# Kernel tuning notes

Measured on AMD Instinct MI355X. Metric: run time of the kernel, lower is better.

Reference implementation:

```python
import jax, jax.numpy as jnp
import numpy as np

EMBED = 100
BATCH = 4096
NUM_NEG = 256
U, P, W, RP, B, C = 30000, 50000, 100000, 50000, 5000, 1000


def _tab(k, v, e=EMBED):
    r = 0.5 / e
    w = jax.random.uniform(k, (v + 1, e), minval=-r, maxval=r, dtype=jnp.float32)
    return w.at[-1].set(0.0)  # padding row is zeros, as in torch code


def setup_inputs() -> dict:
    key = jax.random.key(0)
    ks = jax.random.split(key, 10)
    inp = {
        'user_emb': _tab(ks[0], U),
        'product_emb': _tab(ks[1], P),
        'word_emb': _tab(ks[2], W),
        'brand_emb': _tab(ks[3], B),
        'category_emb': _tab(ks[4], C),
        'rproduct_emb': _tab(ks[5], RP),
        'rel_vecs': jax.random.uniform(ks[6], (8, EMBED), minval=-0.5 / EMBED, maxval=0.5 / EMBED, dtype=jnp.float32),
        'purchase_bias': jnp.zeros((P + 1,), jnp.float32),
        'mentions_bias': jnp.zeros((W + 1,), jnp.float32),
        'describe_bias': jnp.zeros((W + 1,), jnp.float32),
        'produced_bias': jnp.zeros((B + 1,), jnp.float32),
        'belongs_bias': jnp.zeros((C + 1,), jnp.float32),
        'also_bought_bias': jnp.zeros((RP + 1,), jnp.float32),
        'also_viewed_bias': jnp.zeros((RP + 1,), jnp.float32),
        'together_bias': jnp.zeros((RP + 1,), jnp.float32),
    }
    # batch_idxs columns: (u, p, w, b, c, rp1, rp2, rp3), each in its own vocab range
    col_max = [U, P, W, B, C, RP, RP, RP]
    cols = [jax.random.randint(jax.random.fold_in(ks[7], i), (BATCH,), 0, m) for i, m in enumerate(col_max)]
    inp['batch_idxs'] = jnp.stack(cols, axis=1)
    # deterministic stand-in for torch.multinomial negative sampling, one row per relation
    neg_max = [P, W, W, B, C, RP, RP, RP]
    negs = [jax.random.randint(jax.random.fold_in(ks[8], i), (NUM_NEG,), 0, m) for i, m in enumerate(neg_max)]
    inp['neg_idxs'] = jnp.stack(negs, axis=0)
    return inp


def _neg_loss(head_tab, tail_tab, rvec, bias_tab, h, t, n):
    hv = head_tab[h]                      # [B,E] gather
    ex = hv + rvec                        # [B,E]
    tv = tail_tab[t]                      # [B,E]
    bias = bias_tab[t]                    # [B]
    pos = jnp.sum(ex * tv, axis=-1) + bias  # bmm([B,1,E],[B,E,1]) == rowwise dot
    nv = tail_tab[n]                      # [N,E]
    neg = jnp.einsum('be,ne->bn', ex, nv) + bias[:, None]  # [B,N]
    pos_loss = -jax.nn.log_sigmoid(pos)   # == -log(sigmoid(pos)), stable
    neg_loss = -jax.nn.log_sigmoid(-neg).sum(axis=1)
    return (pos_loss + neg_loss).mean()


def reference(batch_idxs, neg_idxs, user_emb, product_emb, word_emb, brand_emb,
              category_emb, rproduct_emb, rel_vecs, purchase_bias, mentions_bias,
              describe_bias, produced_bias, belongs_bias, also_bought_bias,
              also_viewed_bias, together_bias):
    # (head_tab, tail_tab, bias_tab, head_col, tail_col) per relation, in original order
    rels = [
        (user_emb, product_emb, purchase_bias, 0, 1),
        (user_emb, word_emb, mentions_bias, 0, 2),
        (product_emb, word_emb, describe_bias, 1, 2),
        (product_emb, brand_emb, produced_bias, 1, 3),
        (product_emb, category_emb, belongs_bias, 1, 4),
        (product_emb, rproduct_emb, also_bought_bias, 1, 5),
        (product_emb, rproduct_emb, also_viewed_bias, 1, 6),
        (product_emb, rproduct_emb, together_bias, 1, 7),
    ]
    loss = jnp.float32(0.0)
    for r, (ht, tt, bt, hc, tc) in enumerate(rels):
        loss = loss + _neg_loss(ht, tt, rel_vecs[r], bt,
                                batch_idxs[:, hc], batch_idxs[:, tc], neg_idxs[r])
    return loss
```

## Files before the change

### kernel.cpp

```cpp
#include <hip/hip_runtime.h>


#define EMBED   100
#define BATCH   4096
#define NUM_NEG 256
#define BM      64
#define BN      128
#define PITCH   104

typedef __attribute__((ext_vector_type(8))) short s8;
typedef __attribute__((ext_vector_type(4))) float f4;

struct RelP {
    const float* head;
    const float* tail;
    const float* bias;
    int hc, tc;
};

struct Params {
    RelP rel[8];
    const float* rel_vecs;
    const int*   batch_idxs;
    const int*   neg_idxs;
    float*       out;
};

__device__ __forceinline__ float softplus_f(float x) {
    float e = __expf(-fabsf(x));
    return fmaxf(x, 0.0f) + __logf(1.0f + e);
}

__device__ __forceinline__ unsigned short bf16_rne(float f) {
    unsigned u = __float_as_uint(f);
    u += 0x7FFFu + ((u >> 16) & 1u);
    return (unsigned short)(u >> 16);
}

__device__ __forceinline__ float bf16_to_f(short s) {
    return __uint_as_float(((unsigned)(unsigned short)s) << 16);
}

__device__ __forceinline__ s8 pack8(float4 f0, float4 f1) {
    s8 v = { (short)bf16_rne(f0.x), (short)bf16_rne(f0.y),
             (short)bf16_rne(f0.z), (short)bf16_rne(f0.w),
             (short)bf16_rne(f1.x), (short)bf16_rne(f1.y),
             (short)bf16_rne(f1.z), (short)bf16_rne(f1.w) };
    return v;
}

__launch_bounds__(256, 4)
__global__ void ke_kernel(Params p) {
    const int bid = blockIdx.x;
    const int r   = bid & 7;
    const int x   = bid >> 3;
    const int rb  = x & 63;
    const int nb  = x >> 6;
    const int tid = threadIdx.x;

    __shared__ __align__(16) short As[BM * PITCH];
    __shared__ __align__(16) short Bs[BN * PITCH];

    const RelP rp = p.rel[r];

    if (tid < BM) {
        const int row  = tid;
        const int grow = rb * BM + row;
        const int h  = p.batch_idxs[grow * 8 + rp.hc];
        const int ti = p.batch_idxs[grow * 8 + rp.tc];
        const float4* s4p = (const float4*)(rp.head + (size_t)h * EMBED);
        const float4* rv4 = (const float4*)(p.rel_vecs + r * EMBED);
        const unsigned short extra = bf16_rne(rp.bias[ti]);
        short* dst = As + row * PITCH;
#pragma unroll
        for (int c = 0; c < 12; ++c) {
            float4 f0 = s4p[2 * c];
            float4 f1 = s4p[2 * c + 1];
            const float4 a = rv4[2 * c];
            const float4 b = rv4[2 * c + 1];
            f0.x += a.x; f0.y += a.y; f0.z += a.z; f0.w += a.w;
            f1.x += b.x; f1.y += b.y; f1.z += b.z; f1.w += b.w;
            *(s8*)(dst + 8 * c) = pack8(f0, f1);
        }
        {
            float4 f = s4p[24];
            const float4 a = rv4[24];
            f.x += a.x; f.y += a.y; f.z += a.z; f.w += a.w;
            s8 v = { (short)bf16_rne(f.x), (short)bf16_rne(f.y),
                     (short)bf16_rne(f.z), (short)bf16_rne(f.w),
                     (short)extra, 0, 0, 0 };
            *(s8*)(dst + 96) = v;
        }
    } else if (tid < 192) {
        const int row = tid - 64;
        const int n = p.neg_idxs[r * NUM_NEG + nb * BN + row];
        const float4* s4p = (const float4*)(rp.tail + (size_t)n * EMBED);
        short* dst = Bs + row * PITCH;
#pragma unroll
        for (int c = 0; c < 12; ++c) {
            float4 f0 = s4p[2 * c];
            float4 f1 = s4p[2 * c + 1];
            *(s8*)(dst + 8 * c) = pack8(f0, f1);
        }
        {
            float4 f = s4p[24];
            s8 v = { (short)bf16_rne(f.x), (short)bf16_rne(f.y),
                     (short)bf16_rne(f.z), (short)bf16_rne(f.w),
                     (short)0x3F80, 0, 0, 0 };
            *(s8*)(dst + 96) = v;
        }
    }

    const bool doPos = tid >= 128;
    const float* ptail = rp.tail;
    float pbias = 0.0f;
    if (doPos) {
        const int pl   = tid - 128;
        const int prow = rb * BM + nb * 32 + (pl >> 2);
        const int pt   = p.batch_idxs[prow * 8 + rp.tc];
        ptail = rp.tail + (size_t)pt * EMBED;
        pbias = rp.bias[pt];
    }

    __syncthreads();

    const int wave = tid >> 6;
    const int lane = tid & 63;
    const int li   = lane & 15;
    const int q    = lane >> 4;
    const int wm   = wave >> 1;
    const int wn   = wave & 1;

    f4 acc[2][4];
#pragma unroll
    for (int i = 0; i < 2; ++i)
#pragma unroll
        for (int j = 0; j < 4; ++j)
            acc[i][j] = (f4){0.f, 0.f, 0.f, 0.f};

    const short* Ab = As + (wm * 32 + li) * PITCH;
    const short* Bb = Bs + (wn * 64 + li) * PITCH;

#pragma unroll
    for (int s = 0; s < 3; ++s) {
        const int co = 8 * (q + 4 * s);
        s8 a[2], b[4];
        a[0] = *(const s8*)(Ab + co);
        a[1] = *(const s8*)(Ab + 16 * PITCH + co);
        b[0] = *(const s8*)(Bb + co);
        b[1] = *(const s8*)(Bb + 16 * PITCH + co);
        b[2] = *(const s8*)(Bb + 32 * PITCH + co);
        b[3] = *(const s8*)(Bb + 48 * PITCH + co);
#pragma unroll
        for (int i = 0; i < 2; ++i)
#pragma unroll
            for (int j = 0; j < 4; ++j)
                acc[i][j] = __builtin_amdgcn_mfma_f32_16x16x32_bf16(a[i], b[j], acc[i][j], 0, 0, 0);
    }
    {
        const s8 z = {0, 0, 0, 0, 0, 0, 0, 0};
        s8 a[2], b[4];
        a[0] = *(const s8*)(Ab + 96);
        a[1] = *(const s8*)(Ab + 16 * PITCH + 96);
        b[0] = *(const s8*)(Bb + 96);
        b[1] = *(const s8*)(Bb + 16 * PITCH + 96);
        b[2] = *(const s8*)(Bb + 32 * PITCH + 96);
        b[3] = *(const s8*)(Bb + 48 * PITCH + 96);
        b[0] = q ? z : b[0];
        b[1] = q ? z : b[1];
        b[2] = q ? z : b[2];
        b[3] = q ? z : b[3];
#pragma unroll
        for (int i = 0; i < 2; ++i)
#pragma unroll
            for (int j = 0; j < 4; ++j)
                acc[i][j] = __builtin_amdgcn_mfma_f32_16x16x32_bf16(a[i], b[j], acc[i][j], 0, 0, 0);
    }

    float local = 0.0f;
#pragma unroll
    for (int i = 0; i < 2; ++i)
#pragma unroll
        for (int j = 0; j < 4; ++j) {
            local += softplus_f(acc[i][j].x);
            local += softplus_f(acc[i][j].y);
            local += softplus_f(acc[i][j].z);
            local += softplus_f(acc[i][j].w);
        }

    if (doPos) {
        const int pl   = tid - 128;
        const int prl  = pl >> 2;
        const int part = pl & 3;
        const short* exr = As + (nb * 32 + prl) * PITCH;
        const float4* tv = (const float4*)ptail;
        float d0 = 0.f, d1 = 0.f, d2 = 0.f, d3 = 0.f;
        const int cbase = 3 * part;
#pragma unroll
        for (int k = 0; k < 3; ++k) {
            const int c = cbase + k;
            const s8 e = *(const s8*)(exr + 8 * c);
            const float4 t0 = tv[2 * c];
            const float4 t1 = tv[2 * c + 1];
            d0 = fmaf(bf16_to_f(e[0]), t0.x, d0);
            d1 = fmaf(bf16_to_f(e[1]), t0.y, d1);
            d2 = fmaf(bf16_to_f(e[2]), t0.z, d2);
            d3 = fmaf(bf16_to_f(e[3]), t0.w, d3);
            d0 = fmaf(bf16_to_f(e[4]), t1.x, d0);
            d1 = fmaf(bf16_to_f(e[5]), t1.y, d1);
            d2 = fmaf(bf16_to_f(e[6]), t1.z, d2);
            d3 = fmaf(bf16_to_f(e[7]), t1.w, d3);
        }
        if (part == 3) {
            const s8 e = *(const s8*)(exr + 96);
            const float4 t0 = tv[24];
            d0 = fmaf(bf16_to_f(e[0]), t0.x, d0);
            d1 = fmaf(bf16_to_f(e[1]), t0.y, d1);
            d2 = fmaf(bf16_to_f(e[2]), t0.z, d2);
            d3 = fmaf(bf16_to_f(e[3]), t0.w, d3);
        }
        float d = (d0 + d1) + (d2 + d3);
        d += __shfl_xor(d, 1, 64);
        d += __shfl_xor(d, 2, 64);
        if (part == 0) local += softplus_f(-(d + pbias));
    }

#pragma unroll
    for (int off = 32; off > 0; off >>= 1)
        local += __shfl_down(local, off, 64);

    __syncthreads();
    float* wsum = (float*)Bs;
    if ((tid & 63) == 0) wsum[tid >> 6] = local;
    __syncthreads();
    if (tid == 0) {
        const float s = (wsum[0] + wsum[1]) + (wsum[2] + wsum[3]);
        atomicAdd(p.out, s * (1.0f / BATCH));
    }
}

extern "C" void kernel_launch(void* const* d_in, const int* in_sizes, int n_in,
                              void* d_out, int out_size, void* d_ws, size_t ws_size,
                              hipStream_t stream) {
    const float* user  = (const float*)d_in[0];
    const float* prod  = (const float*)d_in[1];
    const float* word  = (const float*)d_in[2];
    const float* brand = (const float*)d_in[3];
    const float* cat   = (const float*)d_in[4];
    const float* rprod = (const float*)d_in[5];

    Params p;
    p.rel_vecs   = (const float*)d_in[6];
    p.batch_idxs = (const int*)d_in[15];
    p.neg_idxs   = (const int*)d_in[16];
    p.out        = (float*)d_out;

    p.rel[0] = {user, prod,  (const float*)d_in[7],  0, 1};
    p.rel[1] = {user, word,  (const float*)d_in[8],  0, 2};
    p.rel[2] = {prod, word,  (const float*)d_in[9],  1, 2};
    p.rel[3] = {prod, brand, (const float*)d_in[10], 1, 3};
    p.rel[4] = {prod, cat,   (const float*)d_in[11], 1, 4};
    p.rel[5] = {prod, rprod, (const float*)d_in[12], 1, 5};
    p.rel[6] = {prod, rprod, (const float*)d_in[13], 1, 6};
    p.rel[7] = {prod, rprod, (const float*)d_in[14], 1, 7};

    hipMemsetAsync(d_out, 0, sizeof(float), stream);
    ke_kernel<<<1024, 256, 0, stream>>>(p);
}
```

Before: 153.8 us.

## Cover all negatives per block and spread gather loads across all threads

Each block now handles all 256 negative samples for its 64-row batch tile (BN 256, grid halved to 512). This removes the duplicate gather and conversion of the head rows across the two former column blocks. The global-to-LDS gather is restructured so all 256 threads participate, with 8 threads per row each loading float4 chunks, instead of one thread per row serially loading 100 floats. The positive-score dot product is spread across all threads in 4-way groups. The trade-offs are a larger accumulator per wave (16 MFMA tiles), fewer blocks resident (launch bounds 2), and more LDS per block.

Result: no change. 152.2 us (median of 2 runs) (-1.0%).

```diff
diff --git a/kernel.cpp b/kernel.cpp
--- a/kernel.cpp
+++ b/kernel.cpp
@@ -5,10 +5,11 @@
 #define BATCH   4096
 #define NUM_NEG 256
 #define BM      64
-#define BN      128
+#define BN      256
 #define PITCH   104
 
 typedef __attribute__((ext_vector_type(8))) short s8;
+typedef __attribute__((ext_vector_type(4))) short s4;
 typedef __attribute__((ext_vector_type(4))) float f4;
 
 struct RelP {
@@ -41,21 +42,17 @@
     return __uint_as_float(((unsigned)(unsigned short)s) << 16);
 }
 
-__device__ __forceinline__ s8 pack8(float4 f0, float4 f1) {
-    s8 v = { (short)bf16_rne(f0.x), (short)bf16_rne(f0.y),
-             (short)bf16_rne(f0.z), (short)bf16_rne(f0.w),
-             (short)bf16_rne(f1.x), (short)bf16_rne(f1.y),
-             (short)bf16_rne(f1.z), (short)bf16_rne(f1.w) };
+__device__ __forceinline__ s4 pack4(float4 f) {
+    s4 v = { (short)bf16_rne(f.x), (short)bf16_rne(f.y),
+             (short)bf16_rne(f.z), (short)bf16_rne(f.w) };
     return v;
 }
 
-__launch_bounds__(256, 4)
+__launch_bounds__(256, 2)
 __global__ void ke_kernel(Params p) {
     const int bid = blockIdx.x;
     const int r   = bid & 7;
-    const int x   = bid >> 3;
-    const int rb  = x & 63;
-    const int nb  = x >> 6;
+    const int rb  = bid >> 3;
     const int tid = threadIdx.x;
 
     __shared__ __align__(16) short As[BM * PITCH];
@@ -63,26 +60,28 @@
 
     const RelP rp = p.rel[r];
 
-    if (tid < BM) {
-        const int row  = tid;
+    const int g    = tid & 7;
+    const int rloc = tid >> 3;
+
+    const float4* rv4 = (const float4*)(p.rel_vecs + r * EMBED);
+#pragma unroll
+    for (int pass = 0; pass < 2; ++pass) {
+        const int row  = pass * 32 + rloc;
         const int grow = rb * BM + row;
-        const int h  = p.batch_idxs[grow * 8 + rp.hc];
-        const int ti = p.batch_idxs[grow * 8 + rp.tc];
+        const int h = p.batch_idxs[grow * 8 + rp.hc];
         const float4* s4p = (const float4*)(rp.head + (size_t)h * EMBED);
-        const float4* rv4 = (const float4*)(p.rel_vecs + r * EMBED);
-        const unsigned short extra = bf16_rne(rp.bias[ti]);
         short* dst = As + row * PITCH;
 #pragma unroll
-        for (int c = 0; c < 12; ++c) {
-            float4 f0 = s4p[2 * c];
-            float4 f1 = s4p[2 * c + 1];
-            const float4 a = rv4[2 * c];
-            const float4 b = rv4[2 * c + 1];
-            f0.x += a.x; f0.y += a.y; f0.z += a.z; f0.w += a.w;
-            f1.x += b.x; f1.y += b.y; f1.z += b.z; f1.w += b.w;
-            *(s8*)(dst + 8 * c) = pack8(f0, f1);
-        }
-        {
+        for (int t = 0; t < 3; ++t) {
+            const int j = g + 8 * t;
+            float4 f = s4p[j];
+            const float4 a = rv4[j];
+            f.x += a.x; f.y += a.y; f.z += a.z; f.w += a.w;
+            *(s4*)(dst + 4 * j) = pack4(f);
+        }
+        if (g == 0) {
+            const int ti = p.batch_idxs[grow * 8 + rp.tc];
+            const unsigned short extra = bf16_rne(rp.bias[ti]);
             float4 f = s4p[24];
             const float4 a = rv4[24];
             f.x += a.x; f.y += a.y; f.z += a.z; f.w += a.w;
@@ -91,18 +90,20 @@
                      (short)extra, 0, 0, 0 };
             *(s8*)(dst + 96) = v;
         }
-    } else if (tid < 192) {
-        const int row = tid - 64;
-        const int n = p.neg_idxs[r * NUM_NEG + nb * BN + row];
+    }
+
+#pragma unroll
+    for (int pass = 0; pass < 8; ++pass) {
+        const int row = pass * 32 + rloc;
+        const int n = p.neg_idxs[r * NUM_NEG + row];
         const float4* s4p = (const float4*)(rp.tail + (size_t)n * EMBED);
         short* dst = Bs + row * PITCH;
 #pragma unroll
-        for (int c = 0; c < 12; ++c) {
-            float4 f0 = s4p[2 * c];
-            float4 f1 = s4p[2 * c + 1];
-            *(s8*)(dst + 8 * c) = pack8(f0, f1);
-        }
-        {
+        for (int t = 0; t < 3; ++t) {
+            const int j = g + 8 * t;
+            *(s4*)(dst + 4 * j) = pack4(s4p[j]);
+        }
+        if (g == 0) {
             float4 f = s4p[24];
             s8 v = { (short)bf16_rne(f.x), (short)bf16_rne(f.y),
                      (short)bf16_rne(f.z), (short)bf16_rne(f.w),
@@ -111,16 +112,12 @@
         }
     }
 
-    const bool doPos = tid >= 128;
-    const float* ptail = rp.tail;
-    float pbias = 0.0f;
-    if (doPos) {
-        const int pl   = tid - 128;
-        const int prow = rb * BM + nb * 32 + (pl >> 2);
-        const int pt   = p.batch_idxs[prow * 8 + rp.tc];
-        ptail = rp.tail + (size_t)pt * EMBED;
-        pbias = rp.bias[pt];
-    }
+    const int prow_l = tid >> 2;
+    const int pp     = tid & 3;
+    const int pgrow  = rb * BM + prow_l;
+    const int pt     = p.batch_idxs[pgrow * 8 + rp.tc];
+    const float* ptail = rp.tail + (size_t)pt * EMBED;
+    const float  pbias = rp.bias[pt];
 
     __syncthreads();
 
@@ -131,49 +128,45 @@
     const int wm   = wave >> 1;
     const int wn   = wave & 1;
 
-    f4 acc[2][4];
+    f4 acc[2][8];
 #pragma unroll
     for (int i = 0; i < 2; ++i)
 #pragma unroll
-        for (int j = 0; j < 4; ++j)
+        for (int j = 0; j < 8; ++j)
             acc[i][j] = (f4){0.f, 0.f, 0.f, 0.f};
 
     const short* Ab = As + (wm * 32 + li) * PITCH;
-    const short* Bb = Bs + (wn * 64 + li) * PITCH;
+    const short* Bb = Bs + (wn * 128 + li) * PITCH;
 
 #pragma unroll
     for (int s = 0; s < 3; ++s) {
         const int co = 8 * (q + 4 * s);
-        s8 a[2], b[4];
+        s8 a[2], b[8];
         a[0] = *(const s8*)(Ab + co);
         a[1] = *(const s8*)(Ab + 16 * PITCH + co);
-        b[0] = *(const s8*)(Bb + co);
-        b[1] = *(const s8*)(Bb + 16 * PITCH + co);
-        b[2] = *(const s8*)(Bb + 32 * PITCH + co);
-        b[3] = *(const s8*)(Bb + 48 * PITCH + co);
+#pragma unroll
+        for (int j = 0; j < 8; ++j)
+            b[j] = *(const s8*)(Bb + j * 16 * PITCH + co);
 #pragma unroll
         for (int i = 0; i < 2; ++i)
 #pragma unroll
-            for (int j = 0; j < 4; ++j)
+            for (int j = 0; j < 8; ++j)
                 acc[i][j] = __builtin_amdgcn_mfma_f32_16x16x32_bf16(a[i], b[j], acc[i][j], 0, 0, 0);
     }
     {
         const s8 z = {0, 0, 0, 0, 0, 0, 0, 0};
-        s8 a[2], b[4];
+        s8 a[2], b[8];
         a[0] = *(const s8*)(Ab + 96);
         a[1] = *(const s8*)(Ab + 16 * PITCH + 96);
-        b[0] = *(const s8*)(Bb + 96);
-        b[1] = *(const s8*)(Bb + 16 * PITCH + 96);
-        b[2] = *(const s8*)(Bb + 32 * PITCH + 96);
-        b[3] = *(const s8*)(Bb + 48 * PITCH + 96);
-        b[0] = q ? z : b[0];
-        b[1] = q ? z : b[1];
-        b[2] = q ? z : b[2];
-        b[3] = q ? z : b[3];
+#pragma unroll
+        for (int j = 0; j < 8; ++j) {
+            b[j] = *(const s8*)(Bb + j * 16 * PITCH + 96);
+            b[j] = q ? z : b[j];
+        }
 #pragma unroll
         for (int i = 0; i < 2; ++i)
 #pragma unroll
-            for (int j = 0; j < 4; ++j)
+            for (int j = 0; j < 8; ++j)
                 acc[i][j] = __builtin_amdgcn_mfma_f32_16x16x32_bf16(a[i], b[j], acc[i][j], 0, 0, 0);
     }
 
@@ -181,48 +174,39 @@
 #pragma unroll
     for (int i = 0; i < 2; ++i)
 #pragma unroll
-        for (int j = 0; j < 4; ++j) {
+        for (int j = 0; j < 8; ++j) {
             local += softplus_f(acc[i][j].x);
             local += softplus_f(acc[i][j].y);
             local += softplus_f(acc[i][j].z);
             local += softplus_f(acc[i][j].w);
         }
 
-    if (doPos) {
-        const int pl   = tid - 128;
-        const int prl  = pl >> 2;
-        const int part = pl & 3;
-        const short* exr = As + (nb * 32 + prl) * PITCH;
+    {
+        const short* exr = As + prow_l * PITCH;
         const float4* tv = (const float4*)ptail;
         float d0 = 0.f, d1 = 0.f, d2 = 0.f, d3 = 0.f;
-        const int cbase = 3 * part;
-#pragma unroll
-        for (int k = 0; k < 3; ++k) {
-            const int c = cbase + k;
-            const s8 e = *(const s8*)(exr + 8 * c);
-            const float4 t0 = tv[2 * c];
-            const float4 t1 = tv[2 * c + 1];
-            d0 = fmaf(bf16_to_f(e[0]), t0.x, d0);
-            d1 = fmaf(bf16_to_f(e[1]), t0.y, d1);
-            d2 = fmaf(bf16_to_f(e[2]), t0.z, d2);
-            d3 = fmaf(bf16_to_f(e[3]), t0.w, d3);
-            d0 = fmaf(bf16_to_f(e[4]), t1.x, d0);
-            d1 = fmaf(bf16_to_f(e[5]), t1.y, d1);
-            d2 = fmaf(bf16_to_f(e[6]), t1.z, d2);
-            d3 = fmaf(bf16_to_f(e[7]), t1.w, d3);
-        }
-        if (part == 3) {
-            const s8 e = *(const s8*)(exr + 96);
+#pragma unroll
+        for (int t = 0; t < 6; ++t) {
+            const int j = pp + 4 * t;
+            const s4 e = *(const s4*)(exr + 4 * j);
+            const float4 t0 = tv[j];
+            d0 = fmaf(bf16_to_f(e.x), t0.x, d0);
+            d1 = fmaf(bf16_to_f(e.y), t0.y, d1);
+            d2 = fmaf(bf16_to_f(e.z), t0.z, d2);
+            d3 = fmaf(bf16_to_f(e.w), t0.w, d3);
+        }
+        if (pp == 0) {
+            const s4 e = *(const s4*)(exr + 96);
             const float4 t0 = tv[24];
-            d0 = fmaf(bf16_to_f(e[0]), t0.x, d0);
-            d1 = fmaf(bf16_to_f(e[1]), t0.y, d1);
-            d2 = fmaf(bf16_to_f(e[2]), t0.z, d2);
-            d3 = fmaf(bf16_to_f(e[3]), t0.w, d3);
+            d0 = fmaf(bf16_to_f(e.x), t0.x, d0);
+            d1 = fmaf(bf16_to_f(e.y), t0.y, d1);
+            d2 = fmaf(bf16_to_f(e.z), t0.z, d2);
+            d3 = fmaf(bf16_to_f(e.w), t0.w, d3);
         }
         float d = (d0 + d1) + (d2 + d3);
         d += __shfl_xor(d, 1, 64);
         d += __shfl_xor(d, 2, 64);
-        if (part == 0) local += softplus_f(-(d + pbias));
+        if (pp == 0) local += softplus_f(-(d + pbias));
     }
 
 #pragma unroll
@@ -265,5 +249,5 @@
     p.rel[7] = {prod, rprod, (const float*)d_in[14], 1, 7};
 
     hipMemsetAsync(d_out, 0, sizeof(float), stream);
-    ke_kernel<<<1024, 256, 0, stream>>>(p);
-}
+    ke_kernel<<<512, 256, 0, stream>>>(p);
+}
```
